# Kernel tuning notes

Hardware: AMD Instinct MI355X
Metric: run time of the kernel (lower is better)

## Reference

```python
import jax, jax.numpy as jnp
import numpy as np

MASK_FILL = jnp.float32(-2**32 + 1)

def dice(x, alpha):
    # x: (S, B, F); batch-dim (dim=0) mean/std, unbiased std like torch.std
    avg = x.mean(axis=0)
    std = jnp.std(x, axis=0, ddof=1)
    p = jax.nn.sigmoid((x - avg) / std)
    return x * p + alpha * x * (1.0 - p)

def setup_inputs() -> dict:
    key = jax.random.key(0)
    ks = jax.random.split(key, 12)
    S, B, D = 200, 1024, 128          # seq_len, batch, 2H
    F = 4 * D                          # num_features = 512
    L1, L2 = 80, 40
    inp = {
        "query": jax.random.normal(ks[0], (B, D), jnp.float32),
        "facts": jax.random.normal(ks[1], (S, B, D), jnp.float32),
        "mask": jax.random.randint(ks[2], (S, B), 0, 2).astype(bool),
        "W1": jax.random.normal(ks[3], (F, L1), jnp.float32) / np.sqrt(F),
        "b1": jnp.zeros((L1,), jnp.float32),
        "a1": jnp.zeros((1,), jnp.float32),
        "W2": jax.random.normal(ks[4], (L1, L2), jnp.float32) / np.sqrt(L1),
        "b2": jnp.zeros((L2,), jnp.float32),
        "a2": jnp.zeros((1,), jnp.float32),
        "W3": jax.random.normal(ks[5], (L2, 1), jnp.float32) / np.sqrt(L2),
        "b3": jnp.zeros((1,), jnp.float32),
    }
    return inp

def reference(query, facts, mask, W1, b1, a1, W2, b2, a2, W3, b3):
    S, B, D = facts.shape
    # faithful to torch: tile along feature dim then reshape (permutes elements)
    q2 = jnp.tile(query, (1, S)).reshape(S, B, D)
    x = jnp.concatenate([q2, facts, q2 * facts, q2 - facts], axis=-1)  # (S,B,4D)
    h = dice(jnp.einsum('sbf,fl->sbl', x, W1) + b1, a1)
    h = dice(jnp.einsum('sbf,fl->sbl', h, W2) + b2, a2)
    logits = (jnp.einsum('sbf,fl->sbl', h, W3) + b3).squeeze(-1)  # (S,B)
    masked = jnp.where(mask, logits, MASK_FILL)
    normalized = jax.nn.softmax(masked, axis=0)
    return normalized[..., None] * facts  # (S,B,D)
```

## Files before the change

### kernel.cpp

```cpp
#include <hip/hip_runtime.h>
#include <hip/hip_bf16.h>
#include <math.h>

#define SS 200
#define BB 1024
#define DD 128
#define FF 512
#define LL1 80
#define LL2 40
#define PP (SS*BB)
#define MASK_FILL_F (-4294967295.0f)
#define NTILE 13

typedef short bf16x8 __attribute__((ext_vector_type(8)));
typedef float f32x4  __attribute__((ext_vector_type(4)));

static __device__ __forceinline__ unsigned short f2bf(float x) {
    __hip_bfloat16 h = __float2bfloat16(x);
    return *reinterpret_cast<unsigned short*>(&h);
}
static __device__ __forceinline__ float bf2f(unsigned short u) {
    __hip_bfloat16 h = *reinterpret_cast<__hip_bfloat16*>(&u);
    return __bfloat162float(h);
}
static __device__ __forceinline__ void split8(const float* x, bf16x8& ah, bf16x8& al) {
#pragma unroll
    for (int j = 0; j < 8; ++j) {
        unsigned u = __float_as_uint(x[j]);
        ah[j] = (short)(u >> 16);
        float hi = __uint_as_float(u & 0xffff0000u);
        al[j] = (short)f2bf(x[j] - hi);
    }
}
static __device__ __forceinline__ float fast_sigmoid(float t) {
    return __builtin_amdgcn_rcpf(1.f + __expf(-t));
}

__global__ void k_prep_all(const float* __restrict__ W1, const float* __restrict__ W2,
                           const unsigned char* __restrict__ mask,
                           const float* __restrict__ query, const float* __restrict__ b1,
                           unsigned short* __restrict__ bfr1,
                           unsigned short* __restrict__ bfr2,
                           float* __restrict__ U, int* __restrict__ flag) {
    const int blk = blockIdx.x;
    if (blk < 20) {
        int t = blk * 256 + threadIdx.x;
        int lane = t & 63;
        int fid  = t >> 6;
        int nt = fid % 5;
        int hl = (fid / 5) % 2;
        int sg = (fid / 10) % 2;
        int kt = fid / 20;
        int n     = nt * 16 + (lane & 15);
        int kbase = kt * 32 + (lane >> 4) * 8;
        unsigned short* o = bfr1 + (size_t)t * 8;
#pragma unroll
        for (int j = 0; j < 8; ++j) {
            int k = kbase + j;
            float w = (sg == 0) ? (W1[(128 + k) * LL1 + n] - W1[(384 + k) * LL1 + n])
                                :  W1[(256 + k) * LL1 + n];
            unsigned short hb = f2bf(w);
            o[j] = (hl == 0) ? hb : f2bf(w - bf2f(hb));
        }
    } else if (blk < 25) {
        int t = (blk - 20) * 256 + threadIdx.x;
        if (t >= 18 * 64) return;
        int lane = t & 63;
        int fid  = t >> 6;
        int hl   = fid & 1;
        int nt   = (fid >> 1) % 3;
        int kt   = fid / 6;
        int n  = nt * 16 + (lane & 15);
        int kb = kt * 32 + (lane >> 4) * 8;
        unsigned short* o = bfr2 + (size_t)t * 8;
#pragma unroll
        for (int j = 0; j < 8; ++j) {
            int k = kb + j;
            float w = (k < LL1 && n < LL2) ? W2[k * LL2 + n] : 0.f;
            unsigned short hb = f2bf(w);
            o[j] = (hl == 0) ? hb : f2bf(w - bf2f(hb));
        }
    } else if (blk == 25) {
        if (threadIdx.x < 64) {
            const uchar4 u = ((const uchar4*)mask)[threadIdx.x];
            const bool f = ((u.y | u.z) | u.w) != 0;
            const unsigned long long anyf = __ballot(f);
            if (threadIdx.x == 0) *flag = (anyf != 0ull) ? 1 : 0;
        }
    } else {
        const int tid = threadIdx.x;
        if (tid >= 240) return;
        const int qr = (blk - 26) * 3 + tid / 80;
        const int n  = tid % 80;
        if (qr >= 1024) return;
        const float* q = query + (size_t)qr * DD;
        float acc = b1[n];
#pragma unroll 8
        for (int k = 0; k < DD; ++k)
            acc = fmaf(q[k], W1[k * LL1 + n] + W1[(384 + k) * LL1 + n], acc);
        U[(size_t)qr * LL1 + n] = acc;
    }
}

__global__ __launch_bounds__(256, 2) void k1_mfma(
    const float* __restrict__ query, const float* __restrict__ facts,
    const unsigned short* __restrict__ bfr, const float* __restrict__ U,
    float* __restrict__ z1) {
    const int tid  = threadIdx.x;
    const int lane = tid & 63;
    const int m    = lane & 15;
    const int quad = lane >> 4;
    const int pw   = blockIdx.x * 128 + (tid >> 6) * 32;

    __shared__ __align__(16) unsigned short lbuf[10240];

    f32x4 acc[2][5];
#pragma unroll
    for (int t = 0; t < 2; ++t)
#pragma unroll
        for (int nt = 0; nt < 5; ++nt) acc[t][nt] = (f32x4){0.f, 0.f, 0.f, 0.f};

    int pr[2], qr[2];
#pragma unroll
    for (int t = 0; t < 2; ++t) {
        pr[t] = pw + t * 16 + m;
        qr[t] = pr[t] / SS;
    }

#pragma unroll 1
    for (int kt = 0; kt < 4; ++kt) {
        const int dbase = kt * 32 + quad * 8;
        float q8[2][8], f8[2][8];
#pragma unroll
        for (int t = 0; t < 2; ++t) {
            const float* qp = query + (size_t)qr[t] * DD + dbase;
            const float* fp = facts + (size_t)pr[t] * DD + dbase;
            *(float4*)&q8[t][0] = *(const float4*)qp;
            *(float4*)&q8[t][4] = *(const float4*)(qp + 4);
            *(float4*)&f8[t][0] = *(const float4*)fp;
            *(float4*)&f8[t][4] = *(const float4*)(fp + 4);
        }
        if (kt) __syncthreads();
        {
            const int4* src = (const int4*)bfr + kt * 1280;
#pragma unroll
            for (int it = 0; it < 5; ++it)
                ((int4*)lbuf)[it * 256 + tid] = src[it * 256 + tid];
        }
        __syncthreads();

#pragma unroll
        for (int sg = 0; sg < 2; ++sg) {
            bf16x8 Bh[5], Bl[5];
#pragma unroll
            for (int nt = 0; nt < 5; ++nt) {
                Bh[nt] = *(const bf16x8*)&lbuf[((sg * 2 + 0) * 5 + nt) * 512 + lane * 8];
                Bl[nt] = *(const bf16x8*)&lbuf[((sg * 2 + 1) * 5 + nt) * 512 + lane * 8];
            }
#pragma unroll
            for (int t = 0; t < 2; ++t) {
                float x8[8];
#pragma unroll
                for (int j = 0; j < 8; ++j)
                    x8[j] = (sg == 0) ? f8[t][j] : q8[t][j] * f8[t][j];
                bf16x8 ah, al;
                split8(x8, ah, al);
#pragma unroll
                for (int nt = 0; nt < 5; ++nt) {
                    acc[t][nt] = __builtin_amdgcn_mfma_f32_16x16x32_bf16(ah, Bh[nt], acc[t][nt], 0, 0, 0);
                    acc[t][nt] = __builtin_amdgcn_mfma_f32_16x16x32_bf16(al, Bh[nt], acc[t][nt], 0, 0, 0);
                    acc[t][nt] = __builtin_amdgcn_mfma_f32_16x16x32_bf16(ah, Bl[nt], acc[t][nt], 0, 0, 0);
                }
            }
        }
    }
#pragma unroll
    for (int t = 0; t < 2; ++t)
#pragma unroll
        for (int r = 0; r < 4; ++r) {
            const int p = pw + t * 16 + quad * 4 + r;
            const float* urow = U + (size_t)(p / SS) * LL1;
#pragma unroll
            for (int nt = 0; nt < 5; ++nt) {
                const int n = nt * 16 + m;
                z1[(size_t)p * LL1 + n] = acc[t][nt][r] + urow[n];
            }
        }
}

__global__ __launch_bounds__(512) void k_light(
    const float* __restrict__ z1, const unsigned short* __restrict__ bfr2,
    const float* __restrict__ a1, const float* __restrict__ b2,
    const float* __restrict__ a2, const float* __restrict__ W3,
    const float* __restrict__ b3, const void* __restrict__ mask,
    const int* __restrict__ flag, float* __restrict__ wbufT) {
    const int tid  = threadIdx.x;
    const int w    = tid >> 6;
    const int lane = tid & 63;
    const int m    = lane & 15;
    const int quad = lane >> 4;
    const int b    = blockIdx.x;

    __shared__ __align__(16) float z1f[NTILE * 16 * 81 + 16];
    __shared__ float psum[480], pssq[480];
    __shared__ float smean[LL1], sistd[LL1];
    __shared__ float sw3[LL2];
    __shared__ float red[8];

    {
        for (int i = tid; i < SS * 20; i += 512) {
            const int s = i / 20;
            const int o = i - s * 20;
            float4 v = ((const float4*)z1)[(size_t)(s * BB + b) * 20 + o];
            float* d = &z1f[s * 81 + o * 4];
            d[0] = v.x; d[1] = v.y; d[2] = v.z; d[3] = v.w;
        }
        for (int i = tid; i < 8 * 81 + 16; i += 512) z1f[SS * 81 + i] = 0.f;
    }
    __syncthreads();

    if (tid < 480) {
        const int l = tid % LL1, c = tid / LL1;
        const int s0 = c * 34;
        const int s1 = (s0 + 34 < SS) ? s0 + 34 : SS;
        float sum = 0.f, ssq = 0.f;
        for (int s = s0; s < s1; ++s) {
            float v = z1f[s * 81 + l];
            sum += v;
            ssq = fmaf(v, v, ssq);
        }
        psum[c * LL1 + l] = sum;
        pssq[c * LL1 + l] = ssq;
    }
    __syncthreads();
    if (tid < LL1) {
        float sum = 0.f, ssq = 0.f;
#pragma unroll
        for (int c = 0; c < 6; ++c) {
            sum += psum[c * LL1 + tid];
            ssq += pssq[c * LL1 + tid];
        }
        float mn  = sum * (1.f / SS);
        float var = (ssq - (float)SS * mn * mn) * (1.f / (SS - 1));
        smean[tid] = mn;
        sistd[tid] = rsqrtf(var);
    }
    __syncthreads();

    const float alpha1 = *a1;
    f32x4 acc2[2][3];
#pragma unroll
    for (int t = 0; t < 2; ++t)
#pragma unroll
        for (int nt = 0; nt < 3; ++nt) acc2[t][nt] = (f32x4){0.f, 0.f, 0.f, 0.f};

    int tile[2];
    bool tl[2];
#pragma unroll
    for (int t = 0; t < 2; ++t) {
        tile[t] = t * 8 + w;
        tl[t]   = (tile[t] < NTILE);
    }

#pragma unroll
    for (int kt = 0; kt < 3; ++kt) {
        bf16x8 Bh[3], Bl[3];
#pragma unroll
        for (int nt = 0; nt < 3; ++nt) {
            Bh[nt] = *(const bf16x8*)(bfr2 + (size_t)((kt * 3 + nt) * 2 + 0) * 512 + lane * 8);
            Bl[nt] = *(const bf16x8*)(bfr2 + (size_t)((kt * 3 + nt) * 2 + 1) * 512 + lane * 8);
        }
        const int kb = kt * 32 + quad * 8;
        const bool lv = (kt < 2 || quad < 2);
#pragma unroll
        for (int t = 0; t < 2; ++t) {
            if (!tl[t]) continue;
            float x8[8];
            if (lv) {
                const float* zr = &z1f[(tile[t] * 16 + m) * 81 + kb];
#pragma unroll
                for (int j = 0; j < 8; ++j) {
                    float v  = zr[j];
                    float pp = fast_sigmoid((v - smean[kb + j]) * sistd[kb + j]);
                    x8[j] = v * (alpha1 + (1.f - alpha1) * pp);
                }
            } else {
#pragma unroll
                for (int j = 0; j < 8; ++j) x8[j] = 0.f;
            }
            bf16x8 ah, al;
            split8(x8, ah, al);
#pragma unroll
            for (int nt = 0; nt < 3; ++nt) {
                acc2[t][nt] = __builtin_amdgcn_mfma_f32_16x16x32_bf16(ah, Bh[nt], acc2[t][nt], 0, 0, 0);
                acc2[t][nt] = __builtin_amdgcn_mfma_f32_16x16x32_bf16(al, Bh[nt], acc2[t][nt], 0, 0, 0);
                acc2[t][nt] = __builtin_amdgcn_mfma_f32_16x16x32_bf16(ah, Bl[nt], acc2[t][nt], 0, 0, 0);
            }
        }
    }
    __syncthreads();

    {
        float b2v[3];
#pragma unroll
        for (int nt = 0; nt < 3; ++nt) {
            const int n = nt * 16 + m;
            b2v[nt] = (n < LL2) ? b2[n] : 0.f;
        }
#pragma unroll
        for (int t = 0; t < 2; ++t) {
            if (!tl[t]) continue;
#pragma unroll
            for (int r = 0; r < 4; ++r) {
                const int srow = tile[t] * 16 + quad * 4 + r;
                if (srow >= SS) continue;
#pragma unroll
                for (int nt = 0; nt < 3; ++nt) {
                    const int n = nt * 16 + m;
                    if (n < LL2) z1f[srow * 41 + n] = acc2[t][nt][r] + b2v[nt];
                }
            }
        }
    }
    __syncthreads();

    if (tid < 480) {
        const int l = tid % LL2, c = tid / LL2;
        const int s0 = c * 17;
        const int s1 = (s0 + 17 < SS) ? s0 + 17 : SS;
        float sum = 0.f, ssq = 0.f;
        for (int s = s0; s < s1; ++s) {
            float v = z1f[s * 41 + l];
            sum += v;
            ssq = fmaf(v, v, ssq);
        }
        psum[c * LL2 + l] = sum;
        pssq[c * LL2 + l] = ssq;
    }
    __syncthreads();
    if (tid < LL2) {
        float sum = 0.f, ssq = 0.f;
#pragma unroll
        for (int c = 0; c < 12; ++c) {
            sum += psum[c * LL2 + tid];
            ssq += pssq[c * LL2 + tid];
        }
        float mn  = sum * (1.f / SS);
        float var = (ssq - (float)SS * mn * mn) * (1.f / (SS - 1));
        smean[tid] = mn;
        sistd[tid] = rsqrtf(var);
        sw3[tid]   = W3[tid];
    }
    __syncthreads();

    const float alpha2 = *a2;
    const int boolLayout = *flag;
    float logit = -3.0e38f;
    if (tid < SS) {
        float dot = b3[0];
#pragma unroll
        for (int k = 0; k < LL2; ++k) {
            float v  = z1f[tid * 41 + k];
            float pp = fast_sigmoid((v - smean[k]) * sistd[k]);
            float hh = v * (pp + alpha2 * (1.f - pp));
            dot = fmaf(hh, sw3[k], dot);
        }
        const int mi = tid * BB + b;
        const bool mk = boolLayout ? (((const unsigned char*)mask)[mi] != 0)
                                   : (((const int*)mask)[mi] != 0);
        logit = mk ? dot : MASK_FILL_F;
    }
    float v = logit;
#pragma unroll
    for (int off = 1; off < 64; off <<= 1) v = fmaxf(v, __shfl_xor(v, off, 64));
    if (lane == 0) red[w] = v;
    __syncthreads();
    float smax = red[0];
#pragma unroll
    for (int i = 1; i < 8; ++i) smax = fmaxf(smax, red[i]);
    __syncthreads();
    const float e = (tid < SS) ? __expf(logit - smax) : 0.f;
    v = e;
#pragma unroll
    for (int off = 1; off < 64; off <<= 1) v += __shfl_xor(v, off, 64);
    if (lane == 0) red[w] = v;
    __syncthreads();
    float ssum = red[0];
#pragma unroll
    for (int i = 1; i < 8; ++i) ssum += red[i];
    const float inv = __builtin_amdgcn_rcpf(ssum);
    if (tid < SS) wbufT[(size_t)b * SS + tid] = e * inv;
}

__global__ __launch_bounds__(256) void k4_scale(
    const float* __restrict__ wbufT, const float* __restrict__ facts,
    float* __restrict__ out) {
    int i = blockIdx.x * 256 + threadIdx.x;
    int p = i >> 5;
    float w = wbufT[(size_t)(p & (BB - 1)) * SS + (p >> 10)];
    float4 f = ((const float4*)facts)[i];
    float4 o;
    o.x = f.x * w; o.y = f.y * w; o.z = f.z * w; o.w = f.w * w;
    ((float4*)out)[i] = o;
}

extern "C" void kernel_launch(void* const* d_in, const int* in_sizes, int n_in,
                              void* d_out, int out_size, void* d_ws, size_t ws_size,
                              hipStream_t stream) {
    const float* query = (const float*)d_in[0];
    const float* facts = (const float*)d_in[1];
    const void*  mask  = d_in[2];
    const float* W1 = (const float*)d_in[3];
    const float* b1 = (const float*)d_in[4];
    const float* a1 = (const float*)d_in[5];
    const float* W2 = (const float*)d_in[6];
    const float* b2 = (const float*)d_in[7];
    const float* a2 = (const float*)d_in[8];
    const float* W3 = (const float*)d_in[9];
    const float* b3 = (const float*)d_in[10];
    float* out = (float*)d_out;

    float* z1 = out;
    float* U  = out + 24600000;
    unsigned short* bfr1 = (unsigned short*)(out + 24739840);
    unsigned short* bfr2 = (unsigned short*)(out + 24801280);
    float* wbufT = (float*)d_ws;
    int*   flag  = (int*)((char*)d_ws + 900 * 1024);

    k_prep_all<<<368, 256, 0, stream>>>(W1, W2, (const unsigned char*)mask,
                                        query, b1, bfr1, bfr2, U, flag);
    k1_mfma<<<PP / 128, 256, 0, stream>>>(query, facts, bfr1, U, z1);
    k_light<<<BB, 512, 0, stream>>>(z1, bfr2, a1, b2, a2, W3, b3, mask, flag, wbufT);
    k4_scale<<<(PP * DD) / (256 * 4), 256, 0, stream>>>(wbufT, facts, out);
}
```

Measured before the change: 298.9 us.

## Stage full W1 fragment in LDS once and prefetch next K-slice activations

The k1_mfma kernel now copies all four K-tiles of the bf16 split weights into shared memory (80KB) up front with a single barrier, instead of reloading one tile per iteration with two barriers each. It also software-pipelines the global loads of query/facts for the next K-slice while the current slice's MFMAs run. This removes the per-iteration syncthreads and hides global latency, but the larger LDS footprint (80KB per block) may reduce occupancy below the launch-bound target of 2 blocks per CU, and the extra prefetch registers raise register pressure.

```diff
diff --git a/kernel.cpp b/kernel.cpp
--- a/kernel.cpp
+++ b/kernel.cpp
@@ -112,7 +112,7 @@
     const int quad = lane >> 4;
     const int pw   = blockIdx.x * 128 + (tid >> 6) * 32;
 
-    __shared__ __align__(16) unsigned short lbuf[10240];
+    __shared__ __align__(16) unsigned short lbuf[40960];
 
     f32x4 acc[2][5];
 #pragma unroll
@@ -127,10 +127,16 @@
         qr[t] = pr[t] / SS;
     }
 
-#pragma unroll 1
-    for (int kt = 0; kt < 4; ++kt) {
-        const int dbase = kt * 32 + quad * 8;
-        float q8[2][8], f8[2][8];
+    {
+        const int4* src = (const int4*)bfr;
+        int4* dst = (int4*)lbuf;
+#pragma unroll 5
+        for (int it = 0; it < 20; ++it)
+            dst[it * 256 + tid] = src[it * 256 + tid];
+    }
+    float q8[2][8], f8[2][8];
+    {
+        const int dbase = quad * 8;
 #pragma unroll
         for (int t = 0; t < 2; ++t) {
             const float* qp = query + (size_t)qr[t] * DD + dbase;
@@ -140,22 +146,32 @@
             *(float4*)&f8[t][0] = *(const float4*)fp;
             *(float4*)&f8[t][4] = *(const float4*)(fp + 4);
         }
-        if (kt) __syncthreads();
-        {
-            const int4* src = (const int4*)bfr + kt * 1280;
-#pragma unroll
-            for (int it = 0; it < 5; ++it)
-                ((int4*)lbuf)[it * 256 + tid] = src[it * 256 + tid];
-        }
-        __syncthreads();
-
+    }
+    __syncthreads();
+
+#pragma unroll 1
+    for (int kt = 0; kt < 4; ++kt) {
+        float qn[2][8], fn[2][8];
+        if (kt < 3) {
+            const int dbase = (kt + 1) * 32 + quad * 8;
+#pragma unroll
+            for (int t = 0; t < 2; ++t) {
+                const float* qp = query + (size_t)qr[t] * DD + dbase;
+                const float* fp = facts + (size_t)pr[t] * DD + dbase;
+                *(float4*)&qn[t][0] = *(const float4*)qp;
+                *(float4*)&qn[t][4] = *(const float4*)(qp + 4);
+                *(float4*)&fn[t][0] = *(const float4*)fp;
+                *(float4*)&fn[t][4] = *(const float4*)(fp + 4);
+            }
+        }
+        const unsigned short* cb = lbuf + kt * 10240;
 #pragma unroll
         for (int sg = 0; sg < 2; ++sg) {
             bf16x8 Bh[5], Bl[5];
 #pragma unroll
             for (int nt = 0; nt < 5; ++nt) {
-                Bh[nt] = *(const bf16x8*)&lbuf[((sg * 2 + 0) * 5 + nt) * 512 + lane * 8];
-                Bl[nt] = *(const bf16x8*)&lbuf[((sg * 2 + 1) * 5 + nt) * 512 + lane * 8];
+                Bh[nt] = *(const bf16x8*)&cb[((sg * 2 + 0) * 5 + nt) * 512 + lane * 8];
+                Bl[nt] = *(const bf16x8*)&cb[((sg * 2 + 1) * 5 + nt) * 512 + lane * 8];
             }
 #pragma unroll
             for (int t = 0; t < 2; ++t) {
@@ -172,6 +188,15 @@
                     acc[t][nt] = __builtin_amdgcn_mfma_f32_16x16x32_bf16(ah, Bl[nt], acc[t][nt], 0, 0, 0);
                 }
             }
+        }
+        if (kt < 3) {
+#pragma unroll
+            for (int t = 0; t < 2; ++t)
+#pragma unroll
+                for (int j = 0; j < 8; ++j) {
+                    q8[t][j] = qn[t][j];
+                    f8[t][j] = fn[t][j];
+                }
         }
     }
 #pragma unroll
```

Result: no change. 298.3 us (-0.2%).
